# Performance work log

Measured on AMD Instinct MI355X. Metric: run time of the kernel, lower is better.

Reference implementation:

```python
import jax, jax.numpy as jnp
import numpy as np

D_MODEL = 1024
NHEAD = 16
HEAD_DIM = D_MODEL // NHEAD
B, T = 2, 2048


def setup_inputs() -> dict:
    key = jax.random.key(0)
    ks = jax.random.split(key, 12)
    s = 1.0 / np.sqrt(D_MODEL)
    return {
        "query": jax.random.normal(ks[0], (B, T, D_MODEL), jnp.float32),
        "key": jax.random.normal(ks[1], (B, T, D_MODEL), jnp.float32),
        "value": jax.random.normal(ks[2], (B, T, D_MODEL), jnp.float32),
        "key_padding_mask": jnp.zeros((B, T), dtype=bool),
        "attn_mask": jnp.zeros((T, T), jnp.float32),
        "stoich_frac": jax.random.uniform(ks[3], (B, T), jnp.float32),
        "Wq": jax.random.uniform(ks[4], (D_MODEL, D_MODEL), jnp.float32, -s, s),
        "bq": jnp.zeros((D_MODEL,), jnp.float32),
        "Wk": jax.random.uniform(ks[5], (D_MODEL, D_MODEL), jnp.float32, -s, s),
        "bk": jnp.zeros((D_MODEL,), jnp.float32),
        "Wv": jax.random.uniform(ks[6], (D_MODEL, D_MODEL), jnp.float32, -s, s),
        "bv": jnp.zeros((D_MODEL,), jnp.float32),
        "Wo": jax.random.uniform(ks[7], (D_MODEL, D_MODEL), jnp.float32, -s, s),
        "bo": jnp.zeros((D_MODEL,), jnp.float32),
        "stoich_alpha": jnp.float32(0.1),
    }


def reference(query, key, value, key_padding_mask, attn_mask, stoich_frac,
              Wq, bq, Wk, bk, Wv, bv, Wo, bo, stoich_alpha):
    Bq, Tq, _ = query.shape
    Tk = key.shape[1]
    scale = HEAD_DIM ** -0.5
    # Linear projections (torch Linear: x @ W.T + b), reshape to [B, H, T, Dh]
    Q = (query @ Wq.T + bq).reshape(Bq, Tq, NHEAD, HEAD_DIM).transpose(0, 2, 1, 3)
    K = (key @ Wk.T + bk).reshape(Bq, Tk, NHEAD, HEAD_DIM).transpose(0, 2, 1, 3)
    V = (value @ Wv.T + bv).reshape(Bq, Tk, NHEAD, HEAD_DIM).transpose(0, 2, 1, 3)
    # Scores [B, H, Tq, Tk]
    scores = jnp.einsum("bhqd,bhkd->bhqk", Q, K) * scale
    # Stoichiometric pairwise bias (T_q == T_k path)
    diff = stoich_frac[:, :, None] - stoich_frac[:, None, :]  # [B, Tq, Tk]
    bias = stoich_alpha * (jnp.log1p(jnp.abs(diff)) * jnp.sign(diff))
    scores = scores + bias[:, None, :, :]
    scores = scores + attn_mask  # broadcasts [Tq, Tk]
    scores = jnp.where(key_padding_mask[:, None, None, :], -jnp.inf, scores)
    probs = jax.nn.softmax(scores, axis=-1)
    # dropout: eval mode / p=0 -> identity
    out = jnp.einsum("bhqk,bhkd->bhqd", probs, V)
    out = out.transpose(0, 2, 1, 3).reshape(Bq, Tq, D_MODEL)
    return out @ Wo.T + bo
```

## Files before the change

### kernel.cpp

```cpp
#include <hip/hip_runtime.h>
#include <math.h>

typedef __bf16 bf16_t;
typedef __bf16 bf16x8 __attribute__((ext_vector_type(8)));
typedef __bf16 bf16x4 __attribute__((ext_vector_type(4)));
typedef float  f32x4  __attribute__((ext_vector_type(4)));

#define NHEAD 16
#define HDIM 64
#define DMODEL 1024
#define TSEQ 2048
#define WEL (DMODEL * DMODEL)

#define SBAR() __builtin_amdgcn_s_barrier()
#define SCHED0() __builtin_amdgcn_sched_barrier(0)
#define LGKM0() do { asm volatile("s_waitcnt lgkmcnt(0)" ::: "memory"); \
                     __builtin_amdgcn_sched_barrier(0); } while (0)

__device__ __forceinline__ f32x4 mfma16(bf16x8 a, bf16x8 b, f32x4 c) {
  return __builtin_amdgcn_mfma_f32_16x16x32_bf16(a, b, c, 0, 0, 0);
}

__device__ __forceinline__ void gload16(const bf16_t* g, bf16_t* l) {
  __builtin_amdgcn_global_load_lds((const __attribute__((address_space(1))) void*)g,
                                   (__attribute__((address_space(3))) void*)l, 16, 0, 0);
}

__device__ __forceinline__ unsigned pk2(float lo, float hi) {
  unsigned short a = __builtin_bit_cast(unsigned short, (__bf16)lo);
  unsigned short c = __builtin_bit_cast(unsigned short, (__bf16)hi);
  return ((unsigned)c << 16) | a;
}

__device__ __forceinline__ void cvtstore(f32x4 x0, f32x4 x1, bf16_t* dh, bf16_t* dl, int off) {
  bf16x8 hfr, lfr;
#pragma unroll
  for (int j = 0; j < 4; ++j) {
    float v = x0[j];
    __bf16 hb = (__bf16)v;
    hfr[j] = hb; lfr[j] = (__bf16)(v - (float)hb);
    float w = x1[j];
    __bf16 wb = (__bf16)w;
    hfr[4 + j] = wb; lfr[4 + j] = (__bf16)(w - (float)wb);
  }
  *(bf16x8*)(dh + off) = hfr;
  *(bf16x8*)(dl + off) = lfr;
}

__global__ __launch_bounds__(256)
void presplit_w(const float* __restrict__ w0, const float* __restrict__ w1,
                const float* __restrict__ w2, const float* __restrict__ w3,
                bf16_t* __restrict__ out) {
  const int y = blockIdx.y;
  const float* src = (y == 0) ? w0 : (y == 1) ? w1 : (y == 2) ? w2 : w3;
  size_t i = ((size_t)blockIdx.x * 256 + threadIdx.x) * 8;
  f32x4 a = *(const f32x4*)(src + i);
  f32x4 c = *(const f32x4*)(src + i + 4);
  bf16x8 h, l;
#pragma unroll
  for (int j = 0; j < 4; ++j) {
    __bf16 hb = (__bf16)a[j];
    h[j] = hb; l[j] = (__bf16)(a[j] - (float)hb);
    __bf16 cb = (__bf16)c[j];
    h[4 + j] = cb; l[4 + j] = (__bf16)(c[j] - (float)cb);
  }
  bf16_t* dh = out + (size_t)y * 2 * WEL;
  *(bf16x8*)(dh + i) = h;
  *(bf16x8*)(dh + WEL + i) = l;
}

__global__ __launch_bounds__(256)
void build_bias(const float* __restrict__ amask, const unsigned char* __restrict__ kpm,
                const float* __restrict__ sf, const float* __restrict__ alpha_p,
                bf16_t* __restrict__ BM) {
  size_t idx = (size_t)blockIdx.x * 256 + threadIdx.x;
  int k8 = (int)(idx & (TSEQ / 8 - 1));
  size_t bq = idx >> 8;
  int b = (int)(bq >> 11);
  int q = (int)(bq & (TSEQ - 1));
  const float sfq = sf[bq];
  const float alpha = *alpha_p;
  const float* sfk = sf + (size_t)b * TSEQ + k8 * 8;
  const float* am  = amask + (size_t)q * TSEQ + k8 * 8;
  const unsigned char* kp = kpm + (size_t)b * TSEQ + k8 * 8;
  bf16x8 o;
#pragma unroll
  for (int j = 0; j < 8; ++j) {
    float df = sfq - sfk[j];
    float v = alpha * copysignf(log1pf(fabsf(df)), df) + am[j];
    if (kp[j]) v = -1.0e30f;
    o[j] = (__bf16)v;
  }
  *(bf16x8*)&BM[idx * 8] = o;
}

template<int MODE>
__global__ __launch_bounds__(512)
void gemm_qkv(const float* __restrict__ A, const bf16_t* __restrict__ Wh,
              const bf16_t* __restrict__ Wl, const float* __restrict__ bias,
              bf16_t* __restrict__ obh, bf16_t* __restrict__ obl) {
  __shared__ bf16_t AH[8 * 512], AL[8 * 512], WHs[2][4 * 512], WLs[2][4 * 512];
  const int tid = threadIdx.x;
  const int lane = tid & 63;
  const int a15 = lane & 15, g = lane >> 4;
  const int wv = tid >> 6, wm = wv >> 1, wn = wv & 1;
  const int m0 = blockIdx.y * 128, n0 = blockIdx.x * 64;
  f32x4 acc[2][2] = {};

  const int t0 = tid >> 6, l0 = tid & 63;
  const float* pA = A + (size_t)(m0 + t0 * 16 + (l0 & 15)) * DMODEL + 8 * (l0 >> 4);
  const int wts = wv & 3;
  const bf16_t* pWg = ((wv < 4) ? Wh : Wl) + (size_t)(n0 + wts * 16 + a15) * DMODEL + 8 * g;

  f32x4 rAa = *(const f32x4*)pA, rAb = *(const f32x4*)(pA + 4);
  gload16(pWg, (wv < 4) ? &WHs[0][wts * 512] : &WLs[0][wts * 512]);

  constexpr int NK = DMODEL / 32;
  for (int t = 0; t < NK; ++t) {
    const int cur = t & 1;
    SBAR();
    cvtstore(rAa, rAb, AH, AL, tid * 8);
    SCHED0();
    if (t + 1 < NK) {
      pA += 32;
      rAa = *(const f32x4*)pA; rAb = *(const f32x4*)(pA + 4);
      SCHED0();
      gload16(pWg + (t + 1) * 32, (wv < 4) ? &WHs[cur ^ 1][wts * 512]
                                           : &WLs[cur ^ 1][wts * 512]);
      SCHED0();
      asm volatile("s_waitcnt vmcnt(3)" ::: "memory");
    } else {
      asm volatile("s_waitcnt vmcnt(0)" ::: "memory");
    }
    LGKM0();
    SBAR();

    bf16x8 ah[2], al[2], wh[2], wl[2];
#pragma unroll
    for (int i = 0; i < 2; ++i) {
      ah[i] = *(const bf16x8*)&AH[(wm * 2 + i) * 512 + lane * 8];
      al[i] = *(const bf16x8*)&AL[(wm * 2 + i) * 512 + lane * 8];
      wh[i] = *(const bf16x8*)&WHs[cur][(wn * 2 + i) * 512 + lane * 8];
      wl[i] = *(const bf16x8*)&WLs[cur][(wn * 2 + i) * 512 + lane * 8];
    }
    __builtin_amdgcn_s_setprio(1);
    if (MODE == 2) {
#pragma unroll
      for (int i = 0; i < 2; ++i)
#pragma unroll
        for (int j = 0; j < 2; ++j) {
          acc[i][j] = mfma16(wh[i], ah[j], acc[i][j]);
          acc[i][j] = mfma16(wh[i], al[j], acc[i][j]);
          acc[i][j] = mfma16(wl[i], ah[j], acc[i][j]);
        }
    } else {
#pragma unroll
      for (int i = 0; i < 2; ++i)
#pragma unroll
        for (int j = 0; j < 2; ++j) {
          acc[i][j] = mfma16(ah[i], wh[j], acc[i][j]);
          acc[i][j] = mfma16(ah[i], wl[j], acc[i][j]);
          acc[i][j] = mfma16(al[i], wh[j], acc[i][j]);
        }
    }
    __builtin_amdgcn_s_setprio(0);
  }

  if (MODE == 1) {
#pragma unroll
    for (int i = 0; i < 2; ++i)
#pragma unroll
      for (int j = 0; j < 2; ++j) {
        int n = n0 + wn * 32 + j * 16 + a15;
        float bs = bias[n];
        int hh = n >> 6, d = n & 63;
#pragma unroll
        for (int r = 0; r < 4; ++r) {
          int m = m0 + wm * 32 + i * 16 + 4 * g + r;
          int bb = m >> 11, t = m & (TSEQ - 1);
          float v = acc[i][j][r] + bs;
          size_t o = (((size_t)(bb * NHEAD + hh)) * TSEQ + t) * HDIM + d;
          __bf16 hb = (__bf16)v;
          obh[o] = hb;
          obl[o] = (__bf16)(v - (float)hb);
        }
      }
  } else {
#pragma unroll
    for (int i = 0; i < 2; ++i)
#pragma unroll
      for (int j = 0; j < 2; ++j) {
        int m = m0 + wm * 32 + j * 16 + a15;
        int bb = m >> 11, t = m & (TSEQ - 1);
#pragma unroll
        for (int r = 0; r < 4; ++r) {
          int n = n0 + wn * 32 + i * 16 + 4 * g + r;
          float v = acc[i][j][r] + bias[n];
          int hh = n >> 6, d = n & 63;
          size_t o = (((size_t)(bb * NHEAD + hh)) * HDIM + d) * TSEQ + t;
          __bf16 hb = (__bf16)v;
          obh[o] = hb;
          obl[o] = (__bf16)(v - (float)hb);
        }
      }
  }
}

__global__ __launch_bounds__(512)
void gemm_out(const bf16_t* __restrict__ Ah, const bf16_t* __restrict__ Al,
              const bf16_t* __restrict__ Wh, const bf16_t* __restrict__ Wl,
              const float* __restrict__ bias, float* __restrict__ of) {
  __shared__ bf16_t AHs[2][8 * 512], ALs[2][8 * 512], WHs[2][4 * 512], WLs[2][4 * 512];
  const int tid = threadIdx.x;
  const int lane = tid & 63;
  const int a15 = lane & 15, g = lane >> 4;
  const int wv = tid >> 6, wm = wv >> 1, wn = wv & 1;
  const int m0 = blockIdx.y * 128, n0 = blockIdx.x * 64;
  f32x4 acc[2][2] = {};

  const bf16_t* pAh = Ah + (size_t)(m0 + wv * 16 + a15) * DMODEL + 8 * g;
  const bf16_t* pAl = Al + (size_t)(m0 + wv * 16 + a15) * DMODEL + 8 * g;
  const int wts = wv & 3;
  const bf16_t* pWg = ((wv < 4) ? Wh : Wl) + (size_t)(n0 + wts * 16 + a15) * DMODEL + 8 * g;

  auto stage = [&](int t, int buf) {
    gload16(pAh + t * 32, &AHs[buf][wv * 512]);
    gload16(pAl + t * 32, &ALs[buf][wv * 512]);
    gload16(pWg + t * 32, (wv < 4) ? &WHs[buf][wts * 512] : &WLs[buf][wts * 512]);
  };
  stage(0, 0);

  constexpr int NK = DMODEL / 32;
  for (int t = 0; t < NK; ++t) {
    const int cur = t & 1;
    if (t + 1 < NK) {
      stage(t + 1, cur ^ 1);
      asm volatile("s_waitcnt vmcnt(3)" ::: "memory");
    } else {
      asm volatile("s_waitcnt vmcnt(0)" ::: "memory");
    }
    SCHED0();
    SBAR();

    bf16x8 ah[2], al[2], wh[2], wl[2];
#pragma unroll
    for (int i = 0; i < 2; ++i) {
      ah[i] = *(const bf16x8*)&AHs[cur][(wm * 2 + i) * 512 + lane * 8];
      al[i] = *(const bf16x8*)&ALs[cur][(wm * 2 + i) * 512 + lane * 8];
      wh[i] = *(const bf16x8*)&WHs[cur][(wn * 2 + i) * 512 + lane * 8];
      wl[i] = *(const bf16x8*)&WLs[cur][(wn * 2 + i) * 512 + lane * 8];
    }
    __builtin_amdgcn_s_setprio(1);
#pragma unroll
    for (int i = 0; i < 2; ++i)
#pragma unroll
      for (int j = 0; j < 2; ++j) {
        acc[i][j] = mfma16(ah[i], wh[j], acc[i][j]);
        acc[i][j] = mfma16(ah[i], wl[j], acc[i][j]);
        acc[i][j] = mfma16(al[i], wh[j], acc[i][j]);
      }
    __builtin_amdgcn_s_setprio(0);
    SBAR();
  }

#pragma unroll
  for (int i = 0; i < 2; ++i)
#pragma unroll
    for (int j = 0; j < 2; ++j) {
      int n = n0 + wn * 32 + j * 16 + a15;
      float bs = bias[n];
#pragma unroll
      for (int r = 0; r < 4; ++r) {
        int m = m0 + wm * 32 + i * 16 + 4 * g + r;
        of[(size_t)m * DMODEL + n] = acc[i][j][r] + bs;
      }
    }
}

__global__ __launch_bounds__(512)
void attn_mfma(const bf16_t* __restrict__ Qhi, const bf16_t* __restrict__ Qlo,
               const bf16_t* __restrict__ Khi, const bf16_t* __restrict__ Klo,
               const bf16_t* __restrict__ Vth, const bf16_t* __restrict__ Vtl,
               const bf16_t* __restrict__ BMt,
               bf16_t* __restrict__ Oh, bf16_t* __restrict__ Ol) {
  __shared__ bf16_t KH[2][8 * 512], KL[2][8 * 512], VH[2][8 * 512], VL[2][8 * 512];
  __shared__ bf16_t PS[8 * 512];
  const int tid = threadIdx.x;
  const int lane = tid & 63, wv = tid >> 6;
  const int a15 = lane & 15, g = lane >> 4;
  const int b = blockIdx.z, h = blockIdx.y, q0 = blockIdx.x * 128;
  const int bh = b * NHEAD + h;
  const int qg = q0 + wv * 16 + a15;
  constexpr int NT = TSEQ / 64;

  const bf16_t* Qh_b = Qhi + ((size_t)bh * TSEQ + qg) * HDIM;
  const bf16_t* Ql_b = Qlo + ((size_t)bh * TSEQ + qg) * HDIM;
  const bf16_t* Kh_b = Khi + (size_t)bh * TSEQ * HDIM;
  const bf16_t* Kl_b = Klo + (size_t)bh * TSEQ * HDIM;
  const bf16_t* Vh_b = Vth + (size_t)bh * HDIM * TSEQ;
  const bf16_t* Vl_b = Vtl + (size_t)bh * HDIM * TSEQ;
  const bf16_t* bmrow = BMt + ((size_t)b * TSEQ + qg) * TSEQ;

  bf16x8 qh[2], ql[2];
  qh[0] = *(const bf16x8*)&Qh_b[8 * g];
  qh[1] = *(const bf16x8*)&Qh_b[32 + 8 * g];
  ql[0] = *(const bf16x8*)&Ql_b[8 * g];
  ql[1] = *(const bf16x8*)&Ql_b[32 + 8 * g];

  f32x4 aco[4] = {};
  float m_run = -3.0e38f, l_run = 0.f;
  bf16x4 bmv[4], bmn[4];

  const int ts = wv >> 1, ks = wv & 1;
  auto stage = [&](int k0, int buf) {
    size_t ko = (size_t)(k0 + 16 * ts + a15) * HDIM + 32 * ks + 8 * g;
    gload16(Kh_b + ko, &KH[buf][wv * 512]);
    gload16(Kl_b + ko, &KL[buf][wv * 512]);
    size_t vo = (size_t)(16 * ts + a15) * TSEQ + k0 + 32 * ks + 8 * g;
    gload16(Vh_b + vo, &VH[buf][wv * 512]);
    gload16(Vl_b + vo, &VL[buf][wv * 512]);
  };

#pragma unroll
  for (int mt = 0; mt < 4; ++mt) bmv[mt] = *(const bf16x4*)&bmrow[16 * mt + 4 * g];
  stage(0, 0);

  const int psb = wv * 512 + a15 * 32;
  const int r3 = a15 & 3;

  for (int t = 0; t < NT; ++t) {
    const int cur = t & 1;
    if (t + 1 < NT) {
      const int kn = (t + 1) * 64;
#pragma unroll
      for (int mt = 0; mt < 4; ++mt) bmn[mt] = *(const bf16x4*)&bmrow[kn + 16 * mt + 4 * g];
      stage(kn, cur ^ 1);
      asm volatile("s_waitcnt vmcnt(8)" ::: "memory");
    } else {
      asm volatile("s_waitcnt vmcnt(0)" ::: "memory");
    }
    SCHED0();
    SBAR();

    f32x4 s4[4];
    __builtin_amdgcn_s_setprio(1);
#pragma unroll
    for (int mt = 0; mt < 4; ++mt) {
      bf16x8 k0h = *(const bf16x8*)&KH[cur][(mt * 2 + 0) * 512 + lane * 8];
      bf16x8 k1h = *(const bf16x8*)&KH[cur][(mt * 2 + 1) * 512 + lane * 8];
      bf16x8 k0l = *(const bf16x8*)&KL[cur][(mt * 2 + 0) * 512 + lane * 8];
      bf16x8 k1l = *(const bf16x8*)&KL[cur][(mt * 2 + 1) * 512 + lane * 8];
      f32x4 sa = {};
      sa = mfma16(k0h, qh[0], sa);
      sa = mfma16(k1h, qh[1], sa);
      sa = mfma16(k0h, ql[0], sa);
      sa = mfma16(k1h, ql[1], sa);
      sa = mfma16(k0l, qh[0], sa);
      sa = mfma16(k1l, qh[1], sa);
      s4[mt] = sa;
    }
    __builtin_amdgcn_s_setprio(0);

#pragma unroll
    for (int mt = 0; mt < 4; ++mt)
#pragma unroll
      for (int r = 0; r < 4; ++r)
        s4[mt][r] = fmaf(s4[mt][r], 0.125f, (float)bmv[mt][r]);

    float tmax = -3.0e38f;
#pragma unroll
    for (int mt = 0; mt < 4; ++mt)
#pragma unroll
      for (int r = 0; r < 4; ++r) tmax = fmaxf(tmax, s4[mt][r]);
    tmax = fmaxf(tmax, __shfl_xor(tmax, 16));
    tmax = fmaxf(tmax, __shfl_xor(tmax, 32));
    if (!__all(tmax - m_run <= 8.0f)) {
      float mnew = fmaxf(m_run, tmax);
      float corr = __expf(m_run - mnew);
      l_run *= corr;
#pragma unroll
      for (int dt = 0; dt < 4; ++dt) aco[dt] *= corr;
      m_run = mnew;
    }
    float psum = 0.f;
    unsigned pk01[4], pk23[4];
#pragma unroll
    for (int mt = 0; mt < 4; ++mt) {
      float p0 = __expf(s4[mt][0] - m_run);
      float p1 = __expf(s4[mt][1] - m_run);
      float p2 = __expf(s4[mt][2] - m_run);
      float p3 = __expf(s4[mt][3] - m_run);
      psum += (p0 + p1) + (p2 + p3);
      pk01[mt] = pk2(p0, p1);
      pk23[mt] = pk2(p2, p3);
    }
    psum += __shfl_xor(psum, 16);
    psum += __shfl_xor(psum, 32);
    l_run += psum;

    __builtin_amdgcn_s_setprio(1);
#pragma unroll
    for (int kss = 0; kss < 2; ++kss) {
#pragma unroll
      for (int mh = 0; mh < 2; ++mh) {
        int mt = kss * 2 + mh;
        int phys = ((mh << 1) | (g >> 1)) ^ r3;
        uint2 w2;
        w2.x = pk01[mt];
        w2.y = pk23[mt];
        *(uint2*)&PS[psb + phys * 8 + (g & 1) * 4] = w2;
      }
      LGKM0();
      bf16x8 pf = *(const bf16x8*)&PS[psb + ((g ^ r3) << 3)];
#pragma unroll
      for (int dt = 0; dt < 4; ++dt) {
        bf16x8 vh = *(const bf16x8*)&VH[cur][(dt * 2 + kss) * 512 + lane * 8];
        bf16x8 vl = *(const bf16x8*)&VL[cur][(dt * 2 + kss) * 512 + lane * 8];
        aco[dt] = mfma16(vh, pf, aco[dt]);
        aco[dt] = mfma16(vl, pf, aco[dt]);
      }
    }
    __builtin_amdgcn_s_setprio(0);

    if (t + 1 < NT) {
#pragma unroll
      for (int mt = 0; mt < 4; ++mt) bmv[mt] = bmn[mt];
    }
    SBAR();
  }

  float inv = 1.0f / l_run;
#pragma unroll
  for (int dt = 0; dt < 4; ++dt) {
    f32x4 o = aco[dt] * inv;
    bf16x4 oh, ol;
#pragma unroll
    for (int r = 0; r < 4; ++r) {
      __bf16 hb = (__bf16)o[r];
      oh[r] = hb;
      ol[r] = (__bf16)(o[r] - (float)hb);
    }
    size_t off = ((size_t)b * TSEQ + qg) * DMODEL + h * HDIM + dt * 16 + 4 * g;
    *(bf16x4*)&Oh[off] = oh;
    *(bf16x4*)&Ol[off] = ol;
  }
}

extern "C" void kernel_launch(void* const* d_in, const int* in_sizes, int n_in,
                              void* d_out, int out_size, void* d_ws, size_t ws_size,
                              hipStream_t stream) {
  const float* query = (const float*)d_in[0];
  const float* key = (const float*)d_in[1];
  const float* value = (const float*)d_in[2];
  const unsigned char* kpm = (const unsigned char*)d_in[3];
  const float* amask = (const float*)d_in[4];
  const float* sf = (const float*)d_in[5];
  const float* Wq = (const float*)d_in[6];
  const float* bq = (const float*)d_in[7];
  const float* Wk = (const float*)d_in[8];
  const float* bk = (const float*)d_in[9];
  const float* Wv = (const float*)d_in[10];
  const float* bv = (const float*)d_in[11];
  const float* Wo = (const float*)d_in[12];
  const float* bo = (const float*)d_in[13];
  const float* alpha = (const float*)d_in[14];
  float* out = (float*)d_out;

  const size_t NEL = (size_t)2 * NHEAD * TSEQ * HDIM;
  bf16_t* p = (bf16_t*)d_ws;
  bf16_t* Qh = p;
  bf16_t* Ql = p + NEL;
  bf16_t* Kh = p + 2 * NEL;
  bf16_t* Kl = p + 3 * NEL;
  bf16_t* Vh = p + 4 * NEL;
  bf16_t* Vl = p + 5 * NEL;
  bf16_t* Oh = p + 6 * NEL;
  bf16_t* Ol = p + 7 * NEL;
  bf16_t* BMt = p + 8 * NEL;
  bf16_t* wsp = p + 10 * NEL;
  bf16_t* wqh = wsp + 0 * WEL, *wql = wsp + 1 * WEL;
  bf16_t* wkh = wsp + 2 * WEL, *wkl = wsp + 3 * WEL;
  bf16_t* wvh = wsp + 4 * WEL, *wvl = wsp + 5 * WEL;
  bf16_t* woh = wsp + 6 * WEL, *wol = wsp + 7 * WEL;

  presplit_w<<<dim3(WEL / (256 * 8), 4), dim3(256), 0, stream>>>(Wq, Wk, Wv, Wo, wsp);
  build_bias<<<dim3(4096), dim3(256), 0, stream>>>(amask, kpm, sf, alpha, BMt);

  dim3 gg(16, 32), gb(512);
  gemm_qkv<1><<<gg, gb, 0, stream>>>(query, wqh, wql, bq, Qh, Ql);
  gemm_qkv<1><<<gg, gb, 0, stream>>>(key, wkh, wkl, bk, Kh, Kl);
  gemm_qkv<2><<<gg, gb, 0, stream>>>(value, wvh, wvl, bv, Vh, Vl);
  dim3 ga(TSEQ / 128, NHEAD, 2);
  attn_mfma<<<ga, gb, 0, stream>>>(Qh, Ql, Kh, Kl, Vh, Vl, BMt, Oh, Ol);
  gemm_out<<<gg, gb, 0, stream>>>(Oh, Ol, woh, wol, bo, out);
}
```

Before: 347.2 us.

## Split Q/K/V weights in-GEMM, merge prep kernels, swizzle block order

The QKV projection GEMMs now read fp32 weights directly and split them into bf16 hi/lo in registers before storing them to LDS. This replaces the separate presplit pass for Wq/Wk/Wv and its async global->LDS double-buffered weight loads. Only Wo is still pre-split, and that work is fused with the bias/mask build into one prep kernel, cutting a launch and the weight-split traffic. Block indices in the GEMMs and attention are remapped with an XCD-style swizzle to improve L2 locality. The trade-offs are more conversion work inside each GEMM tile, fp32 weight reads at double the bytes, and loss of the weight double-buffering.

```diff
diff --git a/kernel.cpp b/kernel.cpp
--- a/kernel.cpp
+++ b/kernel.cpp
@@ -48,32 +48,27 @@
 }
 
 __global__ __launch_bounds__(256)
-void presplit_w(const float* __restrict__ w0, const float* __restrict__ w1,
-                const float* __restrict__ w2, const float* __restrict__ w3,
-                bf16_t* __restrict__ out) {
-  const int y = blockIdx.y;
-  const float* src = (y == 0) ? w0 : (y == 1) ? w1 : (y == 2) ? w2 : w3;
-  size_t i = ((size_t)blockIdx.x * 256 + threadIdx.x) * 8;
-  f32x4 a = *(const f32x4*)(src + i);
-  f32x4 c = *(const f32x4*)(src + i + 4);
-  bf16x8 h, l;
-#pragma unroll
-  for (int j = 0; j < 4; ++j) {
-    __bf16 hb = (__bf16)a[j];
-    h[j] = hb; l[j] = (__bf16)(a[j] - (float)hb);
-    __bf16 cb = (__bf16)c[j];
-    h[4 + j] = cb; l[4 + j] = (__bf16)(c[j] - (float)cb);
-  }
-  bf16_t* dh = out + (size_t)y * 2 * WEL;
-  *(bf16x8*)(dh + i) = h;
-  *(bf16x8*)(dh + WEL + i) = l;
-}
-
-__global__ __launch_bounds__(256)
-void build_bias(const float* __restrict__ amask, const unsigned char* __restrict__ kpm,
-                const float* __restrict__ sf, const float* __restrict__ alpha_p,
-                bf16_t* __restrict__ BM) {
-  size_t idx = (size_t)blockIdx.x * 256 + threadIdx.x;
+void prep(const float* __restrict__ amask, const unsigned char* __restrict__ kpm,
+          const float* __restrict__ sf, const float* __restrict__ alpha_p,
+          bf16_t* __restrict__ BM, const float* __restrict__ Wo,
+          bf16_t* __restrict__ woh, bf16_t* __restrict__ wol) {
+  if (blockIdx.x < 512) {
+    size_t i = ((size_t)blockIdx.x * 256 + threadIdx.x) * 8;
+    f32x4 a = *(const f32x4*)(Wo + i);
+    f32x4 c = *(const f32x4*)(Wo + i + 4);
+    bf16x8 h, l;
+#pragma unroll
+    for (int j = 0; j < 4; ++j) {
+      __bf16 hb = (__bf16)a[j];
+      h[j] = hb; l[j] = (__bf16)(a[j] - (float)hb);
+      __bf16 cb = (__bf16)c[j];
+      h[4 + j] = cb; l[4 + j] = (__bf16)(c[j] - (float)cb);
+    }
+    *(bf16x8*)(woh + i) = h;
+    *(bf16x8*)(wol + i) = l;
+    return;
+  }
+  size_t idx = (size_t)(blockIdx.x - 512) * 256 + threadIdx.x;
   int k8 = (int)(idx & (TSEQ / 8 - 1));
   size_t bq = idx >> 8;
   int b = (int)(bq >> 11);
@@ -96,41 +91,39 @@
 
 template<int MODE>
 __global__ __launch_bounds__(512)
-void gemm_qkv(const float* __restrict__ A, const bf16_t* __restrict__ Wh,
-              const bf16_t* __restrict__ Wl, const float* __restrict__ bias,
-              bf16_t* __restrict__ obh, bf16_t* __restrict__ obl) {
-  __shared__ bf16_t AH[8 * 512], AL[8 * 512], WHs[2][4 * 512], WLs[2][4 * 512];
+void gemm_mfma(const float* __restrict__ A, const float* __restrict__ W,
+               const float* __restrict__ bias,
+               bf16_t* __restrict__ obh, bf16_t* __restrict__ obl) {
+  __shared__ bf16_t AH[8 * 512], AL[8 * 512], WH[4 * 512], WL[4 * 512];
   const int tid = threadIdx.x;
   const int lane = tid & 63;
   const int a15 = lane & 15, g = lane >> 4;
   const int wv = tid >> 6, wm = wv >> 1, wn = wv & 1;
-  const int m0 = blockIdx.y * 128, n0 = blockIdx.x * 64;
+  const unsigned lid = blockIdx.x + 16u * blockIdx.y;
+  const unsigned swz = (lid & 7u) * 64u + (lid >> 3);
+  const int m0 = (int)(swz >> 4) * 128, n0 = (int)(swz & 15u) * 64;
   f32x4 acc[2][2] = {};
 
   const int t0 = tid >> 6, l0 = tid & 63;
-  const float* pA = A + (size_t)(m0 + t0 * 16 + (l0 & 15)) * DMODEL + 8 * (l0 >> 4);
-  const int wts = wv & 3;
-  const bf16_t* pWg = ((wv < 4) ? Wh : Wl) + (size_t)(n0 + wts * 16 + a15) * DMODEL + 8 * g;
-
-  f32x4 rAa = *(const f32x4*)pA, rAb = *(const f32x4*)(pA + 4);
-  gload16(pWg, (wv < 4) ? &WHs[0][wts * 512] : &WLs[0][wts * 512]);
-
-  constexpr int NK = DMODEL / 32;
-  for (int t = 0; t < NK; ++t) {
-    const int cur = t & 1;
-    SBAR();
-    cvtstore(rAa, rAb, AH, AL, tid * 8);
+  const float* pA0 = A + (size_t)(m0 + t0 * 16 + (l0 & 15)) * DMODEL + 8 * (l0 >> 4);
+  const bool doW = (tid < 256);
+  const int sW = tid & 255;
+  const int tw = sW >> 6, lw = sW & 63;
+  const float* pW = W + (size_t)(n0 + tw * 16 + (lw & 15)) * DMODEL + 8 * (lw >> 4);
+
+  f32x4 rA0a = *(const f32x4*)pA0, rA0b = *(const f32x4*)(pA0 + 4);
+  f32x4 rWa = {}, rWb = {};
+  if (doW) { rWa = *(const f32x4*)pW; rWb = *(const f32x4*)(pW + 4); }
+
+  for (int k0 = 0; k0 < DMODEL; k0 += 32) {
+    SBAR();
+    cvtstore(rA0a, rA0b, AH, AL, tid * 8);
+    if (doW) cvtstore(rWa, rWb, WH, WL, sW * 8);
     SCHED0();
-    if (t + 1 < NK) {
-      pA += 32;
-      rAa = *(const f32x4*)pA; rAb = *(const f32x4*)(pA + 4);
-      SCHED0();
-      gload16(pWg + (t + 1) * 32, (wv < 4) ? &WHs[cur ^ 1][wts * 512]
-                                           : &WLs[cur ^ 1][wts * 512]);
-      SCHED0();
-      asm volatile("s_waitcnt vmcnt(3)" ::: "memory");
-    } else {
-      asm volatile("s_waitcnt vmcnt(0)" ::: "memory");
+    if (k0 + 32 < DMODEL) {
+      pA0 += 32;
+      rA0a = *(const f32x4*)pA0; rA0b = *(const f32x4*)(pA0 + 4);
+      if (doW) { pW += 32; rWa = *(const f32x4*)pW; rWb = *(const f32x4*)(pW + 4); }
     }
     LGKM0();
     SBAR();
@@ -140,8 +133,8 @@
     for (int i = 0; i < 2; ++i) {
       ah[i] = *(const bf16x8*)&AH[(wm * 2 + i) * 512 + lane * 8];
       al[i] = *(const bf16x8*)&AL[(wm * 2 + i) * 512 + lane * 8];
-      wh[i] = *(const bf16x8*)&WHs[cur][(wn * 2 + i) * 512 + lane * 8];
-      wl[i] = *(const bf16x8*)&WLs[cur][(wn * 2 + i) * 512 + lane * 8];
+      wh[i] = *(const bf16x8*)&WH[(wn * 2 + i) * 512 + lane * 8];
+      wl[i] = *(const bf16x8*)&WL[(wn * 2 + i) * 512 + lane * 8];
     }
     __builtin_amdgcn_s_setprio(1);
     if (MODE == 2) {
@@ -215,7 +208,9 @@
   const int lane = tid & 63;
   const int a15 = lane & 15, g = lane >> 4;
   const int wv = tid >> 6, wm = wv >> 1, wn = wv & 1;
-  const int m0 = blockIdx.y * 128, n0 = blockIdx.x * 64;
+  const unsigned lid = blockIdx.x + 16u * blockIdx.y;
+  const unsigned swz = (lid & 7u) * 64u + (lid >> 3);
+  const int m0 = (int)(swz >> 4) * 128, n0 = (int)(swz & 15u) * 64;
   f32x4 acc[2][2] = {};
 
   const bf16_t* pAh = Ah + (size_t)(m0 + wv * 16 + a15) * DMODEL + 8 * g;
@@ -288,7 +283,11 @@
   const int tid = threadIdx.x;
   const int lane = tid & 63, wv = tid >> 6;
   const int a15 = lane & 15, g = lane >> 4;
-  const int b = blockIdx.z, h = blockIdx.y, q0 = blockIdx.x * 128;
+  const unsigned lid = blockIdx.x + 16u * (blockIdx.y + 16u * blockIdx.z);
+  const unsigned swz = (lid & 7u) * 64u + (lid >> 3);
+  const int q0 = (int)(swz & 15u) * 128;
+  const int h = (int)((swz >> 4) & 15u);
+  const int b = (int)(swz >> 8);
   const int bh = b * NHEAD + h;
   const int qg = q0 + wv * 16 + a15;
   constexpr int NT = TSEQ / 64;
@@ -477,19 +476,15 @@
   bf16_t* Oh = p + 6 * NEL;
   bf16_t* Ol = p + 7 * NEL;
   bf16_t* BMt = p + 8 * NEL;
-  bf16_t* wsp = p + 10 * NEL;
-  bf16_t* wqh = wsp + 0 * WEL, *wql = wsp + 1 * WEL;
-  bf16_t* wkh = wsp + 2 * WEL, *wkl = wsp + 3 * WEL;
-  bf16_t* wvh = wsp + 4 * WEL, *wvl = wsp + 5 * WEL;
-  bf16_t* woh = wsp + 6 * WEL, *wol = wsp + 7 * WEL;
-
-  presplit_w<<<dim3(WEL / (256 * 8), 4), dim3(256), 0, stream>>>(Wq, Wk, Wv, Wo, wsp);
-  build_bias<<<dim3(4096), dim3(256), 0, stream>>>(amask, kpm, sf, alpha, BMt);
+  bf16_t* woh = p + 10 * NEL;
+  bf16_t* wol = p + 10 * NEL + WEL;
+
+  prep<<<dim3(4608), dim3(256), 0, stream>>>(amask, kpm, sf, alpha, BMt, Wo, woh, wol);
 
   dim3 gg(16, 32), gb(512);
-  gemm_qkv<1><<<gg, gb, 0, stream>>>(query, wqh, wql, bq, Qh, Ql);
-  gemm_qkv<1><<<gg, gb, 0, stream>>>(key, wkh, wkl, bk, Kh, Kl);
-  gemm_qkv<2><<<gg, gb, 0, stream>>>(value, wvh, wvl, bv, Vh, Vl);
+  gemm_mfma<1><<<gg, gb, 0, stream>>>(query, Wq, bq, Qh, Ql);
+  gemm_mfma<1><<<gg, gb, 0, stream>>>(key, Wk, bk, Kh, Kl);
+  gemm_mfma<2><<<gg, gb, 0, stream>>>(value, Wv, bv, Vh, Vl);
   dim3 ga(TSEQ / 128, NHEAD, 2);
   attn_mfma<<<ga, gb, 0, stream>>>(Qh, Ql, Kh, Kl, Vh, Vl, BMt, Oh, Ol);
   gemm_out<<<gg, gb, 0, stream>>>(Oh, Ol, woh, wol, bo, out);
```

New measurement: 339.3 us. 2.3% less time.
